# Kernel tuning notes

Measured on AMD Instinct MI355X. Metric: run time of the kernel, lower is better.

The kernel has to match this reference:

```python
import jax, jax.numpy as jnp
import numpy as np

N = 1_000_000          # points
C_IN = 10              # decorated point features
C_OUT = 64             # pillar feature channels
S = 30_000             # number of pillars (segments)
EPS = 1e-3             # BatchNorm1d eps


def setup_inputs() -> dict:
    key = jax.random.key(0)
    ks = jax.random.split(key, 8)
    inputs = jax.random.normal(ks[0], (N, C_IN), dtype=jnp.float32)
    # every pillar gets ~N/S points; sorted, all segments non-empty
    unq_inv = jnp.sort(jnp.arange(N, dtype=jnp.int32) % S)
    W_lin = jax.random.normal(ks[1], (C_OUT, C_IN), dtype=jnp.float32) * 0.3
    gamma = 1.0 + 0.1 * jax.random.normal(ks[2], (C_OUT,), dtype=jnp.float32)
    beta = 0.1 * jax.random.normal(ks[3], (C_OUT,), dtype=jnp.float32)
    dw1 = jax.random.normal(ks[4], (C_OUT,), dtype=jnp.float32) * 0.5      # depthwise 1x1 conv (groups=C)
    pw1 = jax.random.normal(ks[5], (C_OUT, C_OUT), dtype=jnp.float32) * 0.1  # pointwise 1x1 conv
    dw2 = jax.random.normal(ks[6], (C_OUT,), dtype=jnp.float32) * 0.5
    pw2 = jax.random.normal(ks[7], (C_OUT, C_OUT), dtype=jnp.float32) * 0.1
    return {"inputs": inputs, "unq_inv": unq_inv, "W_lin": W_lin,
            "gamma": gamma, "beta": beta, "dw1": dw1, "pw1": pw1,
            "dw2": dw2, "pw2": pw2}


def reference(inputs, unq_inv, W_lin, gamma, beta, dw1, pw1, dw2, pw2):
    # Linear (no bias) -> BN (training-mode batch stats) -> ReLU
    x = inputs @ W_lin.T                                   # [N, C]
    mu = jnp.mean(x, axis=0)
    var = jnp.mean(jnp.square(x - mu), axis=0)             # biased var, as torch BN
    x = (x - mu) * jax.lax.rsqrt(var + EPS) * gamma + beta
    x = jax.nn.relu(x)

    # MAFF attention: local branch (depthwise scale -> swish -> 1x1 conv)
    s = x * dw1                                            # groups=C 1x1 conv == per-channel scale
    xl = (s * jax.nn.sigmoid(s)) @ pw1.T                   # [N, C]
    # global branch: avg-pool over points -> depthwise scale -> relu -> 1x1 conv
    g = jnp.mean(x, axis=0)                                # [C]
    xg = pw2 @ jax.nn.relu(dw2 * g)                        # [C]
    wei = jax.nn.sigmoid(xl + xg)                          # broadcast [N,C] + [C]
    xi = x * (1.0 + wei)

    # segment reductions keyed by pillar id (scatter_max + scatter_sum)
    x_max = jax.ops.segment_max(xi, unq_inv, num_segments=S,
                                indices_are_sorted=True)
    x_sum = jax.ops.segment_sum(xi, unq_inv, num_segments=S,
                                indices_are_sorted=True)
    return x_max + x_sum                                   # [S, C]
```

## Files before the change

kernel.cpp:

```cpp
#include <hip/hip_runtime.h>
#include <math.h>

#define N_PTS   1000000
#define CI      10
#define C       64
#define NSEG    30000
#define BN_EPS  1e-3f


using f32x4 = __attribute__((ext_vector_type(4))) float;
using s16x8 = __attribute__((ext_vector_type(8))) short;

__device__ inline short f2bf(float x) {
    unsigned u = __float_as_uint(x);
    unsigned r = (u + 0x7fffu + ((u >> 16) & 1u)) >> 16;
    return (short)r;
}
__device__ inline unsigned pack_trunc(float lo, float hi) {
    return (__float_as_uint(hi) & 0xffff0000u) | (__float_as_uint(lo) >> 16);
}
__device__ inline float frcp(float x) { return __builtin_amdgcn_rcpf(x); }

__global__ void __launch_bounds__(256) k_moments(const float* __restrict__ inp,
                                                 const int* __restrict__ idx,
                                                 float* __restrict__ ws,
                                                 int* __restrict__ starts) {
    const int tid = threadIdx.x;
    float v[65];
#pragma unroll
    for (int k = 0; k < 65; ++k) v[k] = 0.f;

    for (int p = blockIdx.x * blockDim.x + tid; p < N_PTS; p += gridDim.x * blockDim.x) {
        const float2* r2 = (const float2*)(inp + (size_t)p * CI);
        float2 a0 = r2[0], a1 = r2[1], a2 = r2[2], a3 = r2[3], a4 = r2[4];
        float r[CI] = {a0.x, a0.y, a1.x, a1.y, a2.x, a2.y, a3.x, a3.y, a4.x, a4.y};
#pragma unroll
        for (int i = 0; i < CI; ++i) v[i] += r[i];
        int kk = 10;
#pragma unroll
        for (int i = 0; i < CI; ++i)
#pragma unroll
            for (int j = i; j < CI; ++j) { v[kk] = fmaf(r[i], r[j], v[kk]); ++kk; }

        int iv = idx[p];
        if (p == 0) starts[0] = 0;
        else if (idx[p - 1] != iv) starts[iv] = p;
    }

#pragma unroll
    for (int k = 0; k < 65; ++k) {
#pragma unroll
        for (int off = 32; off >= 1; off >>= 1)
            v[k] += __shfl_xor(v[k], off, 64);
    }
    __shared__ float red[4 * 65];
    const int wv = tid >> 6, ln = tid & 63;
    if (ln == 0) {
#pragma unroll
        for (int k = 0; k < 65; ++k) red[wv * 65 + k] = v[k];
    }
    __syncthreads();
    if (tid < 65)
        atomicAdd(&ws[tid], red[tid] + red[65 + tid] + red[130 + tid] + red[195 + tid]);
}

__global__ void k_finalize(const float* __restrict__ W,
                           const float* __restrict__ gamma,
                           const float* __restrict__ beta,
                           float* __restrict__ ws) {
    const int c = threadIdx.x;
    float w[CI];
#pragma unroll
    for (int i = 0; i < CI; ++i) w[i] = W[c * CI + i];
    const float inv_n = 1.f / (float)N_PTS;

    float mu = 0.f;
#pragma unroll
    for (int i = 0; i < CI; ++i) mu = fmaf(w[i], ws[i], mu);
    mu *= inv_n;

    float ex2 = 0.f;
    int kk = 10;
#pragma unroll
    for (int i = 0; i < CI; ++i)
#pragma unroll
        for (int j = i; j < CI; ++j) {
            float m = ws[kk];
            float t = w[i] * w[j] * m;
            ex2 += (i == j) ? t : 2.f * t;
            ++kk;
        }
    ex2 *= inv_n;

    float var = ex2 - mu * mu;
    float rstd = rsqrtf(var + BN_EPS);
    float a = rstd * gamma[c];
    ws[128 + c] = a;
    ws[192 + c] = beta[c] - mu * a;
#pragma unroll
    for (int i = 0; i < CI; ++i) ws[384 + c * CI + i] = a * w[i];
}

__global__ void __launch_bounds__(256) k_gstats(const float* __restrict__ inp,
                                                float* __restrict__ ws) {
    const int tid  = threadIdx.x;
    const int wv   = tid >> 6;
    const int lane = tid & 63;
    const int m = lane & 15;
    const int q = lane >> 4;

    s16x8 wfr[4];
#pragma unroll
    for (int nt = 0; nt < 4; ++nt) {
        s16x8 t;
#pragma unroll
        for (int j = 0; j < 8; ++j) {
            int k = 8 * q + j;
            t[j] = (k < CI) ? f2bf(ws[384 + (nt * 16 + m) * CI + k]) : (short)0;
        }
        wfr[nt] = t;
    }
    float bb[4];
#pragma unroll
    for (int nt = 0; nt < 4; ++nt) bb[nt] = ws[192 + nt * 16 + m];

    const int wid = blockIdx.x * 4 + wv;
    const int nw  = gridDim.x * 4;
    const int NB  = N_PTS / 16;

    float2 P0, P1, P2, P3;
    auto loadrows = [&](int pb) {
        const float* row = inp + (size_t)(pb + m) * CI;
        if (q == 0) {
            P0 = *(const float2*)(row);     P1 = *(const float2*)(row + 2);
            P2 = *(const float2*)(row + 4); P3 = *(const float2*)(row + 6);
        } else if (q == 1) {
            P0 = *(const float2*)(row + 8);
        }
    };
    P0 = P1 = P2 = P3 = make_float2(0.f, 0.f);

    float sm[4] = {0.f, 0.f, 0.f, 0.f};
    const f32x4 zero = {0.f, 0.f, 0.f, 0.f};

    if (wid < NB) loadrows(wid * 16);
    for (int b = wid; b < NB; b += nw) {
        float2 L0 = P0, L1 = P1, L2 = P2, L3 = P3;
        if (b + nw < NB) loadrows((b + nw) * 16);

        union { s16x8 v; unsigned u[4]; } t;
        t.v = s16x8{0, 0, 0, 0, 0, 0, 0, 0};
        if (q < 2) t.u[0] = pack_trunc(L0.x, L0.y);
        if (q == 0) {
            t.u[1] = pack_trunc(L1.x, L1.y);
            t.u[2] = pack_trunc(L2.x, L2.y);
            t.u[3] = pack_trunc(L3.x, L3.y);
        }

        f32x4 xt[4];
#pragma unroll
        for (int nt = 0; nt < 4; ++nt) {
            xt[nt] = __builtin_amdgcn_mfma_f32_16x16x32_bf16(t.v, wfr[nt], zero, 0, 0, 0);
#pragma unroll
            for (int r = 0; r < 4; ++r)
                sm[nt] += fmaxf(xt[nt][r] + bb[nt], 0.f);
        }
    }

#pragma unroll
    for (int nt = 0; nt < 4; ++nt) {
        sm[nt] += __shfl_xor(sm[nt], 16, 64);
        sm[nt] += __shfl_xor(sm[nt], 32, 64);
    }
    float S = sm[0];
    if (q == 1) S = sm[1];
    if (q == 2) S = sm[2];
    if (q == 3) S = sm[3];

    __shared__ float red[4 * 64];
    red[wv * 64 + lane] = S;
    __syncthreads();
    if (tid < 64)
        atomicAdd(&ws[256 + tid], red[tid] + red[64 + tid] + red[128 + tid] + red[192 + tid]);
}

__global__ void k_xg(const float* __restrict__ dw2,
                     const float* __restrict__ pw2,
                     float* __restrict__ ws) {
    __shared__ float t[C];
    const int c = threadIdx.x;
    float g = ws[256 + c] * (1.f / (float)N_PTS);
    t[c] = fmaxf(dw2[c] * g, 0.f);
    __syncthreads();
    float acc = 0.f;
#pragma unroll
    for (int k = 0; k < C; ++k) acc = fmaf(pw2[c * C + k], t[k], acc);
    ws[320 + c] = acc;
}

#define LD 68
#define SEGW 6
__global__ void __launch_bounds__(128) k_main(const float* __restrict__ inp,
                                              const float* __restrict__ dw1,
                                              const float* __restrict__ pw1,
                                              const float* __restrict__ ws,
                                              const int* __restrict__ starts,
                                              float* __restrict__ out) {
    const int tid  = threadIdx.x;
    const int wv   = tid >> 6;
    const int lane = tid & 63;
    const int m = lane & 15;
    const int q = lane >> 4;

    s16x8 wfr[4];
#pragma unroll
    for (int nt = 0; nt < 4; ++nt) {
        s16x8 t;
#pragma unroll
        for (int j = 0; j < 8; ++j) {
            int k = 8 * q + j;
            t[j] = (k < CI) ? f2bf(ws[384 + (nt * 16 + m) * CI + k]) : (short)0;
        }
        wfr[nt] = t;
    }
    s16x8 bfr[4][2];
#pragma unroll
    for (int nt = 0; nt < 4; ++nt)
#pragma unroll
        for (int kc = 0; kc < 2; ++kc) {
            const float* src = pw1 + (nt * 16 + m) * C + kc * 32 + q * 8;
            float4 p0 = *(const float4*)src;
            float4 p1 = *(const float4*)(src + 4);
            s16x8 t;
            t[0] = f2bf(p0.x); t[1] = f2bf(p0.y); t[2] = f2bf(p0.z); t[3] = f2bf(p0.w);
            t[4] = f2bf(p1.x); t[5] = f2bf(p1.y); t[6] = f2bf(p1.z); t[7] = f2bf(p1.w);
            bfr[nt][kc] = t;
        }

    float bb[4], d1v[4], xgv[4];
#pragma unroll
    for (int nt = 0; nt < 4; ++nt) {
        bb[nt]  = ws[192 + nt * 16 + m];
        d1v[nt] = dw1[nt * 16 + m];
        xgv[nt] = ws[320 + nt * 16 + m];
    }

    __shared__ float sb[2][16 * LD];
    float* my = sb[wv];
    const f32x4 zero = {0.f, 0.f, 0.f, 0.f};

    const int w  = blockIdx.x * 2 + wv;
    const int s0 = w * SEGW;

    int st[SEGW + 1];
#pragma unroll
    for (int i = 0; i <= SEGW; ++i) {
        int s = s0 + i;
        st[i] = (s >= NSEG) ? N_PTS : starts[s];
    }
    const int start   = st[0];
    const int end_all = st[SEGW];

    int cur = s0, nsel = 1;
    int end_cur = st[1];

    float sm[4]  = {0.f, 0.f, 0.f, 0.f};
    float mxv[4] = {-INFINITY, -INFINITY, -INFINITY, -INFINITY};

    auto flushseg = [&](int s) {
#pragma unroll
        for (int nt = 0; nt < 4; ++nt) {
            sm[nt] += __shfl_xor(sm[nt], 16, 64);
            sm[nt] += __shfl_xor(sm[nt], 32, 64);
            mxv[nt] = fmaxf(mxv[nt], __shfl_xor(mxv[nt], 16, 64));
            mxv[nt] = fmaxf(mxv[nt], __shfl_xor(mxv[nt], 32, 64));
        }
        float S = sm[0], M = mxv[0];
        if (q == 1) { S = sm[1]; M = mxv[1]; }
        if (q == 2) { S = sm[2]; M = mxv[2]; }
        if (q == 3) { S = sm[3]; M = mxv[3]; }
        out[(size_t)s * C + lane] = S + M;
#pragma unroll
        for (int nt = 0; nt < 4; ++nt) { sm[nt] = 0.f; mxv[nt] = -INFINITY; }
    };
    auto advance_end = [&]() {
        ++nsel;
        int e = st[1];
        if (nsel >= 2) e = st[2];
        if (nsel >= 3) e = st[3];
        if (nsel >= 4) e = st[4];
        if (nsel >= 5) e = st[5];
        if (nsel >= 6) e = st[6];
        end_cur = e;
    };

    float2 P0, P1, P2, P3;
    auto loadrows = [&](int pb) {
        const float* row = inp + (size_t)min(pb + m, N_PTS - 1) * CI;
        if (q == 0) {
            P0 = *(const float2*)(row);     P1 = *(const float2*)(row + 2);
            P2 = *(const float2*)(row + 4); P3 = *(const float2*)(row + 6);
        } else if (q == 1) {
            P0 = *(const float2*)(row + 8);
        }
    };
    P0 = P1 = P2 = P3 = make_float2(0.f, 0.f);
    loadrows(start);

    for (int base = start; base < end_all; base += 16) {
        float2 L0 = P0, L1 = P1, L2 = P2, L3 = P3;
        if (base + 16 < end_all) loadrows(base + 16);

        const int nb = min(16, end_all - base);

        union { s16x8 v; unsigned u[4]; } t;
        t.v = s16x8{0, 0, 0, 0, 0, 0, 0, 0};
        if (q < 2) t.u[0] = pack_trunc(L0.x, L0.y);
        if (q == 0) {
            t.u[1] = pack_trunc(L1.x, L1.y);
            t.u[2] = pack_trunc(L2.x, L2.y);
            t.u[3] = pack_trunc(L3.x, L3.y);
        }

        f32x4 xt[4];
#pragma unroll
        for (int nt = 0; nt < 4; ++nt)
            xt[nt] = __builtin_amdgcn_mfma_f32_16x16x32_bf16(t.v, wfr[nt], zero, 0, 0, 0);

        float xn[4][4];
#pragma unroll
        for (int nt = 0; nt < 4; ++nt)
#pragma unroll
            for (int r = 0; r < 4; ++r) {
                float x = fmaxf(xt[nt][r] + bb[nt], 0.f);
                xn[nt][r] = x;
                float sg = x * d1v[nt];
                float sw = sg * frcp(1.f + __expf(-sg));
                my[(4 * q + r) * LD + nt * 16 + m] = sw;
            }
        __threadfence_block();

        s16x8 av[2];
#pragma unroll
        for (int kc = 0; kc < 2; ++kc) {
            const float* src = &my[m * LD + kc * 32 + q * 8];
            float4 p0 = *(const float4*)src;
            float4 p1 = *(const float4*)(src + 4);
            union { s16x8 v; unsigned u[4]; } tt;
            tt.u[0] = pack_trunc(p0.x, p0.y);
            tt.u[1] = pack_trunc(p0.z, p0.w);
            tt.u[2] = pack_trunc(p1.x, p1.y);
            tt.u[3] = pack_trunc(p1.z, p1.w);
            av[kc] = tt.v;
        }

        f32x4 xi[4];
#pragma unroll
        for (int nt = 0; nt < 4; ++nt) {
            xi[nt] = __builtin_amdgcn_mfma_f32_16x16x32_bf16(av[0], bfr[nt][0], zero, 0, 0, 0);
            xi[nt] = __builtin_amdgcn_mfma_f32_16x16x32_bf16(av[1], bfr[nt][1], xi[nt], 0, 0, 0);
        }
        __threadfence_block();

#pragma unroll
        for (int nt = 0; nt < 4; ++nt)
#pragma unroll
            for (int r = 0; r < 4; ++r) {
                float v   = xi[nt][r] + xgv[nt];
                float wei = frcp(1.f + __expf(-v));
                float x   = xn[nt][r];
                xi[nt][r] = fmaf(x, wei, x);
            }

        const int fin = base + nb;
        if (fin <= end_cur) {
            if (nb == 16) {
#pragma unroll
                for (int nt = 0; nt < 4; ++nt)
#pragma unroll
                    for (int r = 0; r < 4; ++r) {
                        sm[nt] += xi[nt][r];
                        mxv[nt] = fmaxf(mxv[nt], xi[nt][r]);
                    }
            } else {
#pragma unroll
                for (int nt = 0; nt < 4; ++nt)
#pragma unroll
                    for (int r = 0; r < 4; ++r) {
                        bool act = (4 * q + r) < nb;
                        sm[nt] += act ? xi[nt][r] : 0.f;
                        mxv[nt] = fmaxf(mxv[nt], act ? xi[nt][r] : -INFINITY);
                    }
            }
            if (fin == end_cur) { flushseg(cur); ++cur; advance_end(); }
        } else {
            const int B = end_cur - base;
#pragma unroll
            for (int nt = 0; nt < 4; ++nt)
#pragma unroll
                for (int r = 0; r < 4; ++r) {
                    bool act = (4 * q + r) < B;
                    sm[nt] += act ? xi[nt][r] : 0.f;
                    mxv[nt] = fmaxf(mxv[nt], act ? xi[nt][r] : -INFINITY);
                }
            flushseg(cur); ++cur;
#pragma unroll
            for (int nt = 0; nt < 4; ++nt)
#pragma unroll
                for (int r = 0; r < 4; ++r) {
                    int pt = 4 * q + r;
                    bool act = (pt >= B) && (pt < nb);
                    sm[nt] += act ? xi[nt][r] : 0.f;
                    mxv[nt] = fmaxf(mxv[nt], act ? xi[nt][r] : -INFINITY);
                }
            advance_end();
        }
    }
}

extern "C" void kernel_launch(void* const* d_in, const int* in_sizes, int n_in,
                              void* d_out, int out_size, void* d_ws, size_t ws_size,
                              hipStream_t stream) {
    const float* inp   = (const float*)d_in[0];
    const int*   unq   = (const int*)d_in[1];
    const float* W     = (const float*)d_in[2];
    const float* gamma = (const float*)d_in[3];
    const float* beta  = (const float*)d_in[4];
    const float* dw1   = (const float*)d_in[5];
    const float* pw1   = (const float*)d_in[6];
    const float* dw2   = (const float*)d_in[7];
    const float* pw2   = (const float*)d_in[8];
    float* out = (float*)d_out;
    float* ws  = (float*)d_ws;
    int* starts = (int*)ws + 1024;

    hipMemsetAsync(ws, 0, 384 * sizeof(float), stream);

    k_moments <<<1024, 256, 0, stream>>>(inp, unq, ws, starts);
    k_finalize<<<1,    64,  0, stream>>>(W, gamma, beta, ws);
    k_gstats  <<<512,  256, 0, stream>>>(inp, ws);
    k_xg      <<<1,    64,  0, stream>>>(dw2, pw2, ws);
    k_main    <<<2500, 128, 0, stream>>>(inp, dw1, pw1, ws, starts, out);
}
```

Baseline: 302.3 us.

## Fold finalize and global-branch kernels into neighbours; shrink segments per wave

```diff
diff --git a/kernel.cpp b/kernel.cpp
--- a/kernel.cpp
+++ b/kernel.cpp
@@ -64,44 +64,10 @@
         atomicAdd(&ws[tid], red[tid] + red[65 + tid] + red[130 + tid] + red[195 + tid]);
 }
 
-__global__ void k_finalize(const float* __restrict__ W,
-                           const float* __restrict__ gamma,
-                           const float* __restrict__ beta,
-                           float* __restrict__ ws) {
-    const int c = threadIdx.x;
-    float w[CI];
-#pragma unroll
-    for (int i = 0; i < CI; ++i) w[i] = W[c * CI + i];
-    const float inv_n = 1.f / (float)N_PTS;
-
-    float mu = 0.f;
-#pragma unroll
-    for (int i = 0; i < CI; ++i) mu = fmaf(w[i], ws[i], mu);
-    mu *= inv_n;
-
-    float ex2 = 0.f;
-    int kk = 10;
-#pragma unroll
-    for (int i = 0; i < CI; ++i)
-#pragma unroll
-        for (int j = i; j < CI; ++j) {
-            float m = ws[kk];
-            float t = w[i] * w[j] * m;
-            ex2 += (i == j) ? t : 2.f * t;
-            ++kk;
-        }
-    ex2 *= inv_n;
-
-    float var = ex2 - mu * mu;
-    float rstd = rsqrtf(var + BN_EPS);
-    float a = rstd * gamma[c];
-    ws[128 + c] = a;
-    ws[192 + c] = beta[c] - mu * a;
-#pragma unroll
-    for (int i = 0; i < CI; ++i) ws[384 + c * CI + i] = a * w[i];
-}
-
 __global__ void __launch_bounds__(256) k_gstats(const float* __restrict__ inp,
+                                                const float* __restrict__ W,
+                                                const float* __restrict__ gamma,
+                                                const float* __restrict__ beta,
                                                 float* __restrict__ ws) {
     const int tid  = threadIdx.x;
     const int wv   = tid >> 6;
@@ -109,6 +75,50 @@
     const int m = lane & 15;
     const int q = lane >> 4;
 
+    __shared__ float wp[C * CI];
+    __shared__ float bsh[C];
+
+    if (tid < C) {
+        const int c = tid;
+        float w[CI];
+#pragma unroll
+        for (int i = 0; i < CI; ++i) w[i] = W[c * CI + i];
+        const float inv_n = 1.f / (float)N_PTS;
+
+        float mu = 0.f;
+#pragma unroll
+        for (int i = 0; i < CI; ++i) mu = fmaf(w[i], ws[i], mu);
+        mu *= inv_n;
+
+        float ex2 = 0.f;
+        int kk = 10;
+#pragma unroll
+        for (int i = 0; i < CI; ++i)
+#pragma unroll
+            for (int j = i; j < CI; ++j) {
+                float mm = ws[kk];
+                float t = w[i] * w[j] * mm;
+                ex2 += (i == j) ? t : 2.f * t;
+                ++kk;
+            }
+        ex2 *= inv_n;
+
+        float var = ex2 - mu * mu;
+        float rstd = rsqrtf(var + BN_EPS);
+        float a = rstd * gamma[c];
+        float b = beta[c] - mu * a;
+        bsh[c] = b;
+        ws[128 + c] = a;
+        ws[192 + c] = b;
+#pragma unroll
+        for (int i = 0; i < CI; ++i) {
+            float wi = a * w[i];
+            wp[c * CI + i] = wi;
+            ws[384 + c * CI + i] = wi;
+        }
+    }
+    __syncthreads();
+
     s16x8 wfr[4];
 #pragma unroll
     for (int nt = 0; nt < 4; ++nt) {
@@ -116,13 +126,13 @@
 #pragma unroll
         for (int j = 0; j < 8; ++j) {
             int k = 8 * q + j;
-            t[j] = (k < CI) ? f2bf(ws[384 + (nt * 16 + m) * CI + k]) : (short)0;
+            t[j] = (k < CI) ? f2bf(wp[(nt * 16 + m) * CI + k]) : (short)0;
         }
         wfr[nt] = t;
     }
     float bb[4];
 #pragma unroll
-    for (int nt = 0; nt < 4; ++nt) bb[nt] = ws[192 + nt * 16 + m];
+    for (int nt = 0; nt < 4; ++nt) bb[nt] = bsh[nt * 16 + m];
 
     const int wid = blockIdx.x * 4 + wv;
     const int nw  = gridDim.x * 4;
@@ -184,25 +194,13 @@
         atomicAdd(&ws[256 + tid], red[tid] + red[64 + tid] + red[128 + tid] + red[192 + tid]);
 }
 
-__global__ void k_xg(const float* __restrict__ dw2,
-                     const float* __restrict__ pw2,
-                     float* __restrict__ ws) {
-    __shared__ float t[C];
-    const int c = threadIdx.x;
-    float g = ws[256 + c] * (1.f / (float)N_PTS);
-    t[c] = fmaxf(dw2[c] * g, 0.f);
-    __syncthreads();
-    float acc = 0.f;
-#pragma unroll
-    for (int k = 0; k < C; ++k) acc = fmaf(pw2[c * C + k], t[k], acc);
-    ws[320 + c] = acc;
-}
-
 #define LD 68
-#define SEGW 6
+#define SEGW 2
 __global__ void __launch_bounds__(128) k_main(const float* __restrict__ inp,
                                               const float* __restrict__ dw1,
                                               const float* __restrict__ pw1,
+                                              const float* __restrict__ dw2,
+                                              const float* __restrict__ pw2,
                                               const float* __restrict__ ws,
                                               const int* __restrict__ starts,
                                               float* __restrict__ out) {
@@ -211,6 +209,7 @@
     const int lane = tid & 63;
     const int m = lane & 15;
     const int q = lane >> 4;
+    const f32x4 zero = {0.f, 0.f, 0.f, 0.f};
 
     s16x8 wfr[4];
 #pragma unroll
@@ -242,27 +241,53 @@
     for (int nt = 0; nt < 4; ++nt) {
         bb[nt]  = ws[192 + nt * 16 + m];
         d1v[nt] = dw1[nt * 16 + m];
-        xgv[nt] = ws[320 + nt * 16 + m];
+    }
+
+    {
+        const float inv_n = 1.f / (float)N_PTS;
+        s16x8 axg[2];
+#pragma unroll
+        for (int kc = 0; kc < 2; ++kc) {
+            union { s16x8 v; unsigned u[4]; } t;
+#pragma unroll
+            for (int jj = 0; jj < 4; ++jj) {
+                int k0 = kc * 32 + q * 8 + 2 * jj;
+                float t0 = fmaxf(dw2[k0]     * (ws[256 + k0]     * inv_n), 0.f);
+                float t1 = fmaxf(dw2[k0 + 1] * (ws[256 + k0 + 1] * inv_n), 0.f);
+                t.u[jj] = pack_trunc(t0, t1);
+            }
+            axg[kc] = t.v;
+        }
+#pragma unroll
+        for (int nt = 0; nt < 4; ++nt) {
+            s16x8 b0, b1;
+            const float* src0 = pw2 + (nt * 16 + m) * C + q * 8;
+            const float* src1 = src0 + 32;
+            float4 p0 = *(const float4*)src0, p1 = *(const float4*)(src0 + 4);
+            float4 p2 = *(const float4*)src1, p3 = *(const float4*)(src1 + 4);
+            b0[0] = f2bf(p0.x); b0[1] = f2bf(p0.y); b0[2] = f2bf(p0.z); b0[3] = f2bf(p0.w);
+            b0[4] = f2bf(p1.x); b0[5] = f2bf(p1.y); b0[6] = f2bf(p1.z); b0[7] = f2bf(p1.w);
+            b1[0] = f2bf(p2.x); b1[1] = f2bf(p2.y); b1[2] = f2bf(p2.z); b1[3] = f2bf(p2.w);
+            b1[4] = f2bf(p3.x); b1[5] = f2bf(p3.y); b1[6] = f2bf(p3.z); b1[7] = f2bf(p3.w);
+            f32x4 acc = __builtin_amdgcn_mfma_f32_16x16x32_bf16(axg[0], b0, zero, 0, 0, 0);
+            acc = __builtin_amdgcn_mfma_f32_16x16x32_bf16(axg[1], b1, acc, 0, 0, 0);
+            xgv[nt] = acc[0];
+        }
     }
 
     __shared__ float sb[2][16 * LD];
     float* my = sb[wv];
-    const f32x4 zero = {0.f, 0.f, 0.f, 0.f};
 
     const int w  = blockIdx.x * 2 + wv;
     const int s0 = w * SEGW;
 
-    int st[SEGW + 1];
-#pragma unroll
-    for (int i = 0; i <= SEGW; ++i) {
-        int s = s0 + i;
-        st[i] = (s >= NSEG) ? N_PTS : starts[s];
-    }
-    const int start   = st[0];
-    const int end_all = st[SEGW];
-
-    int cur = s0, nsel = 1;
-    int end_cur = st[1];
+    int st1 = starts[s0 + 1];
+    int st2 = (s0 + 2 < NSEG) ? starts[s0 + 2] : N_PTS;
+    const int start   = starts[s0];
+    const int end_all = st2;
+
+    int cur = s0;
+    int end_cur = st1;
 
     float sm[4]  = {0.f, 0.f, 0.f, 0.f};
     float mxv[4] = {-INFINITY, -INFINITY, -INFINITY, -INFINITY};
@@ -282,16 +307,6 @@
         out[(size_t)s * C + lane] = S + M;
 #pragma unroll
         for (int nt = 0; nt < 4; ++nt) { sm[nt] = 0.f; mxv[nt] = -INFINITY; }
-    };
-    auto advance_end = [&]() {
-        ++nsel;
-        int e = st[1];
-        if (nsel >= 2) e = st[2];
-        if (nsel >= 3) e = st[3];
-        if (nsel >= 4) e = st[4];
-        if (nsel >= 5) e = st[5];
-        if (nsel >= 6) e = st[6];
-        end_cur = e;
     };
 
     float2 P0, P1, P2, P3;
@@ -392,7 +407,7 @@
                         mxv[nt] = fmaxf(mxv[nt], act ? xi[nt][r] : -INFINITY);
                     }
             }
-            if (fin == end_cur) { flushseg(cur); ++cur; advance_end(); }
+            if (fin == end_cur) { flushseg(cur); ++cur; end_cur = st2; }
         } else {
             const int B = end_cur - base;
 #pragma unroll
@@ -413,7 +428,7 @@
                     sm[nt] += act ? xi[nt][r] : 0.f;
                     mxv[nt] = fmaxf(mxv[nt], act ? xi[nt][r] : -INFINITY);
                 }
-            advance_end();
+            end_cur = st2;
         }
     }
 }
@@ -436,9 +451,7 @@
 
     hipMemsetAsync(ws, 0, 384 * sizeof(float), stream);
 
-    k_moments <<<1024, 256, 0, stream>>>(inp, unq, ws, starts);
-    k_finalize<<<1,    64,  0, stream>>>(W, gamma, beta, ws);
-    k_gstats  <<<512,  256, 0, stream>>>(inp, ws);
-    k_xg      <<<1,    64,  0, stream>>>(dw2, pw2, ws);
-    k_main    <<<2500, 128, 0, stream>>>(inp, dw1, pw1, ws, starts, out);
-}
+    k_moments <<<512,  256, 0, stream>>>(inp, unq, ws, starts);
+    k_gstats  <<<512,  256, 0, stream>>>(inp, W, gamma, beta, ws);
+    k_main    <<<7500, 128, 0, stream>>>(inp, dw1, pw1, dw2, pw2, ws, starts, out);
+}
```

Result: slower. 341.9 us (+13.1%).
